# Performance work log

Hardware: AMD Instinct MI355X
Metric: run time of the kernel (lower is better)

Reference implementation:

```python
import jax, jax.numpy as jnp
import numpy as np

EPS = 1e-6
INV_T = 100.0
STEPS = 7  # eval_steps


def setup_inputs() -> dict:
    key = jax.random.key(0)
    k1, k2 = jax.random.split(key)
    B, C, H, W, R = 8, 512, 128, 128, 64
    x = jax.random.uniform(k1, (B, C, H, W), dtype=jnp.float32)
    bases = jax.random.uniform(k2, (B, C, R), dtype=jnp.float32)
    # _build_bases: F.normalize(bases, dim=1) -> L2 normalize over D
    bases = bases / jnp.maximum(jnp.linalg.norm(bases, axis=1, keepdims=True), 1e-12)
    return {"x": x, "bases": bases}


def _nmf(xf, bases):
    # xf: [B, D, N], bases: [B, D, R]
    # coef init: softmax(inv_t * x^T @ bases) over R
    coef = jax.nn.softmax(INV_T * jnp.einsum('bdn,bdr->bnr', xf, bases), axis=-1)

    def step(carry, _):
        bases, coef = carry
        # multiplicative update for coef: coef * (x^T B) / (coef (B^T B))
        num = jnp.einsum('bdn,bdr->bnr', xf, bases)          # [B,N,R]
        den = coef @ (jnp.swapaxes(bases, 1, 2) @ bases)      # [B,N,R]
        coef = coef * num / (den + EPS)
        # multiplicative update for bases: B * (x coef) / (B (coef^T coef))
        num = jnp.einsum('bdn,bnr->bdr', xf, coef)            # [B,D,R]
        den = bases @ (jnp.swapaxes(coef, 1, 2) @ coef)       # [B,D,R]
        bases = bases * num / (den + EPS)
        return (bases, coef), None

    (bases, coef), _ = jax.lax.scan(step, (bases, coef), None, length=STEPS)
    # compute_coef: one final coef update
    num = jnp.einsum('bdn,bdr->bnr', xf, bases)
    den = coef @ (jnp.swapaxes(bases, 1, 2) @ bases)
    coef = coef * num / (den + EPS)
    return bases, coef


def reference(x, bases):
    B, C, H, W = x.shape
    N = H * W
    xf = x.reshape(B, C, N)  # S=1, D=C
    bases, coef = _nmf(xf, bases)
    out = jnp.einsum('bdr,bnr->bdn', bases, coef)  # bases @ coef^T
    return out.reshape(B, C, H, W)
```

## Files before the change

kernel.cpp:

```cpp
#include <hip/hip_runtime.h>
#include <cstdint>
#include <cstddef>

namespace {

constexpr int B_ = 8;
constexpr int D_ = 512;
constexpr int N_ = 16384;
constexpr int R_ = 64;
constexpr float EPS_ = 1e-6f;
constexpr float INVT_ = 100.0f;

typedef __attribute__((ext_vector_type(4))) float f32x4;
typedef __attribute__((ext_vector_type(8))) short s16x8;
typedef __attribute__((ext_vector_type(4))) short s16x4;

#define MFMA16(A, Bv, C) __builtin_amdgcn_mfma_f32_16x16x32_bf16(A, Bv, C, 0, 0, 0)

#define VMW(n) asm volatile("s_waitcnt vmcnt(" #n ")" ::: "memory")
#define LGKM0 asm volatile("s_waitcnt lgkmcnt(0)" ::: "memory")
#define SCHEDB __builtin_amdgcn_sched_barrier(0)
#define BARRIER do { SCHEDB; __builtin_amdgcn_s_barrier(); SCHEDB; } while (0)

typedef __attribute__((address_space(3))) unsigned int lds_u32_t;
typedef const __attribute__((address_space(1))) unsigned int glb_u32_t;

__device__ __forceinline__ void gl2lds16(const void* g, void* l) {
    __builtin_amdgcn_global_load_lds((glb_u32_t*)g, (lds_u32_t*)l, 16, 0, 0);
}

__device__ __forceinline__ unsigned short f2bf(float x) {
    unsigned int u = __float_as_uint(x);
    return (unsigned short)((u + 0x7fffu + ((u >> 16) & 1u)) >> 16);
}
__device__ __forceinline__ float bf2f(unsigned short u) {
    return __uint_as_float(((unsigned int)u) << 16);
}
__device__ __forceinline__ s16x8 ld8(const unsigned short* p) {
    return *reinterpret_cast<const s16x8*>(p);
}

__device__ __forceinline__ void stage16(const unsigned short* __restrict__ rowbase,
        size_t rstride_elems, unsigned short* __restrict__ buf, int w, int lane) {
#pragma unroll
    for (int i = 0; i < 4; ++i) {
        int r = w * 4 + i;
        const char* src = reinterpret_cast<const char*>(rowbase + (size_t)r * rstride_elems)
                        + ((lane << 4) ^ ((r & 7) << 4));
        gl2lds16(src, reinterpret_cast<char*>(buf) + r * 1024);
    }
}
__device__ __forceinline__ s16x8 read_t16(const unsigned short* buf, int row, int ks, int h4) {
    return *reinterpret_cast<const s16x8*>(reinterpret_cast<const char*>(buf)
        + row * 1024 + ((ks * 64 + h4 * 16) ^ ((row & 7) << 4)));
}
__device__ __forceinline__ void stage_c16(const unsigned short* __restrict__ cnr_n0,
        unsigned short* __restrict__ buf, int w, int lane) {
    int h = w & 1;
    int row = h * 8 + (lane >> 3);
    const char* src = reinterpret_cast<const char*>(cnr_n0 + (size_t)row * R_)
                    + ((((lane & 7) ^ (row & 7))) << 4);
    gl2lds16(src, reinterpret_cast<char*>(buf) + h * 1024);
}
__device__ __forceinline__ s16x8 read_c16(const unsigned short* buf, int row, int ks, int h4) {
    return *reinterpret_cast<const s16x8*>(reinterpret_cast<const char*>(buf)
        + row * 128 + ((ks * 64 + h4 * 16) ^ ((row & 7) << 4)));
}
__device__ __forceinline__ float read_c_scalar(const unsigned short* buf, int row, int r) {
    return bf2f(*reinterpret_cast<const unsigned short*>(
        reinterpret_cast<const char*>(buf) + row * 128 + ((r * 2) ^ ((row & 7) << 4))));
}

__global__ __launch_bounds__(256) void k_convert(const float* __restrict__ X,
        unsigned short* __restrict__ Xhi, unsigned short* __restrict__ XThi,
        unsigned short* __restrict__ XTlo, int have_lo) {
    __shared__ float lds[64][65];
    int id = blockIdx.x;
    int nblk = id & 255, dblk = (id >> 8) & 7, b = id >> 11;
    int t = threadIdx.x;
    const float* Xb = X + ((size_t)b * D_ + dblk * 64) * N_ + (size_t)nblk * 64;
    {
        int d = t >> 2;
#pragma unroll
        for (int i = 0; i < 4; ++i) {
            int c = (t & 3) * 4 + i * 16;
            f32x4 v = *reinterpret_cast<const f32x4*>(Xb + (size_t)d * N_ + c);
#pragma unroll
            for (int k = 0; k < 4; ++k) lds[d][c + k] = v[k];
        }
    }
    __syncthreads();
    {
        int d = t >> 2, c0 = (t & 3) * 16;
        unsigned short* dst = Xhi + ((size_t)b * D_ + dblk * 64 + d) * N_ + (size_t)nblk * 64 + c0;
        s16x8 v0, v1;
#pragma unroll
        for (int k = 0; k < 8; ++k) {
            v0[k] = (short)f2bf(lds[d][c0 + k]);
            v1[k] = (short)f2bf(lds[d][c0 + 8 + k]);
        }
        *reinterpret_cast<s16x8*>(dst) = v0;
        *reinterpret_cast<s16x8*>(dst + 8) = v1;
    }
    {
        int n = t >> 2, c0 = (t & 3) * 16;
        size_t off = ((size_t)b * N_ + nblk * 64 + n) * D_ + dblk * 64 + c0;
        s16x8 h0, h1, l0, l1;
#pragma unroll
        for (int k = 0; k < 8; ++k) {
            float a = lds[c0 + k][n], c = lds[c0 + 8 + k][n];
            unsigned short ha = f2bf(a), hc = f2bf(c);
            h0[k] = (short)ha; h1[k] = (short)hc;
            l0[k] = (short)f2bf(a - bf2f(ha));
            l1[k] = (short)f2bf(c - bf2f(hc));
        }
        *reinterpret_cast<s16x8*>(XThi + off) = h0;
        *reinterpret_cast<s16x8*>(XThi + off + 8) = h1;
        if (have_lo) {
            *reinterpret_cast<s16x8*>(XTlo + off) = l0;
            *reinterpret_cast<s16x8*>(XTlo + off + 8) = l1;
        }
    }
}

__global__ __launch_bounds__(256) void k_ginit(const float* __restrict__ Bin,
        float* __restrict__ bases, unsigned short* __restrict__ BThi,
        unsigned short* __restrict__ BTlo) {
    __shared__ float lds[64][65];
    int id = blockIdx.x, dblk = id & 7, b = id >> 3;
    int t = threadIdx.x, tn = t & 63, tq = t >> 6;
    const float* Bb = Bin + ((size_t)b * D_ + dblk * 64) * R_;
    float* bb = bases + ((size_t)b * D_ + dblk * 64) * R_;
#pragma unroll
    for (int i = 0; i < 16; ++i) {
        int d = i * 4 + tq;
        float v = Bb[d * R_ + tn];
        lds[d][tn] = v;
        bb[d * R_ + tn] = v;
    }
    __syncthreads();
#pragma unroll
    for (int i = 0; i < 16; ++i) {
        int r = i * 4 + tq;
        float v = lds[tn][r];
        unsigned short hi = f2bf(v);
        size_t off = ((size_t)b * R_ + r) * D_ + dblk * 64 + tn;
        BThi[off] = hi;
        BTlo[off] = f2bf(v - bf2f(hi));
    }
}

__global__ __launch_bounds__(256) void k_gram(const unsigned short* __restrict__ BT,
        unsigned short* __restrict__ G) {
    int b = blockIdx.x;
    int t = threadIdx.x, lane = t & 63, w = t >> 6;
    int m16 = lane & 15, h4 = lane >> 4;
    const unsigned short* BTb = BT + (size_t)b * R_ * D_;
    f32x4 acc[4];
#pragma unroll
    for (int j = 0; j < 4; ++j) acc[j] = (f32x4){0.f, 0.f, 0.f, 0.f};
#pragma unroll
    for (int k0 = 0; k0 < D_; k0 += 32) {
        int kg = k0 + (h4 << 3);
        s16x8 frag[4];
#pragma unroll
        for (int j = 0; j < 4; ++j)
            frag[j] = ld8(BTb + (size_t)(j * 16 + m16) * D_ + kg);
        s16x8 fw = ld8(BTb + (size_t)(w * 16 + m16) * D_ + kg);
#pragma unroll
        for (int j = 0; j < 4; ++j) acc[j] = MFMA16(fw, frag[j], acc[j]);
    }
    unsigned short* Gb = G + (size_t)b * R_ * R_;
#pragma unroll
    for (int j = 0; j < 4; ++j)
#pragma unroll
        for (int q = 0; q < 4; ++q) {
            int r1 = 16 * w + (h4 << 2) + q;
            Gb[r1 * R_ + 16 * j + m16] = f2bf(acc[j][q]);
        }
}

template <int LO>
__global__ __launch_bounds__(256, 2) void k_init(const unsigned short* __restrict__ XThi,
        const unsigned short* __restrict__ XTlo, const unsigned short* __restrict__ BThi,
        const unsigned short* __restrict__ BTlo, const unsigned short* __restrict__ G,
        unsigned short* __restrict__ CTb, unsigned short* __restrict__ Cnr) {
    __shared__ __align__(16) unsigned short xhbuf[2][16 * 512];
    __shared__ __align__(16) unsigned short xlbuf[LO ? 2 : 1][16 * 512];
    __shared__ __align__(16) unsigned short ldsc[16 * 64];
    __shared__ float red[2][4][16];
    int id = blockIdx.x, blk = id & 63, b = id >> 6;
    int t = threadIdx.x, lane = t & 63, w = t >> 6;
    int m16 = lane & 15, h4 = lane >> 4;
    const unsigned short* XTb = XThi + (size_t)b * N_ * D_;
    const unsigned short* XLb = XTlo + (size_t)b * N_ * D_;
    const unsigned short* BThb = BThi + (size_t)b * R_ * D_;
    const unsigned short* BTlb = BTlo + (size_t)b * R_ * D_;
    const unsigned short* Gb = G + (size_t)b * R_ * R_;
    unsigned short* CTbb = CTb + (size_t)b * R_ * N_;
    unsigned short* Cnrb = Cnr + (size_t)b * N_ * R_;
    s16x8 abh[16], abl[16], g[2];
#pragma unroll
    for (int ks = 0; ks < 16; ++ks) {
        size_t off = (size_t)(w * 16 + m16) * D_ + ks * 32 + h4 * 8;
        abh[ks] = ld8(BThb + off);
        abl[ks] = ld8(BTlb + off);
    }
#pragma unroll
    for (int ks = 0; ks < 2; ++ks)
        g[ks] = ld8(Gb + (size_t)(w * 16 + m16) * R_ + ks * 32 + h4 * 8);
    SCHEDB;
    stage16(XTb + (size_t)(blk * 16 + 0) * 16 * D_, D_, xhbuf[0], w, lane);
    if (LO) stage16(XLb + (size_t)(blk * 16 + 0) * 16 * D_, D_, xlbuf[0], w, lane);
    stage16(XTb + (size_t)(blk * 16 + 1) * 16 * D_, D_, xhbuf[1], w, lane);
    if (LO) stage16(XLb + (size_t)(blk * 16 + 1) * 16 * D_, D_, xlbuf[1], w, lane);
    SCHEDB;

    int swz = (m16 & 7) << 4;
    char* crow = reinterpret_cast<char*>(ldsc) + m16 * 128;

    for (int tt = 0; tt < 16; ++tt) {
        int cur = tt & 1;
        int n0 = (blk * 16 + tt) * 16;
        if (LO) {
            if (tt == 0) VMW(8);
            else if (tt == 15) VMW(5);
            else VMW(13);
        } else {
            if (tt == 0) VMW(4);
            else if (tt == 15) VMW(5);
            else VMW(9);
        }
        BARRIER;
        const unsigned short* xh = xhbuf[cur];
        const unsigned short* xl = xlbuf[LO ? cur : 0];
        f32x4 acc = (f32x4){0.f, 0.f, 0.f, 0.f};
#pragma unroll
        for (int ks = 0; ks < 16; ++ks) {
            s16x8 bh = read_t16(xh, m16, ks, h4);
            acc = MFMA16(abh[ks], bh, acc);
            acc = MFMA16(abl[ks], bh, acc);
            if (LO) {
                s16x8 bl = read_t16(xl, m16, ks, h4);
                acc = MFMA16(abh[ks], bl, acc);
            }
        }
        float mx = fmaxf(fmaxf(acc[0], acc[1]), fmaxf(acc[2], acc[3]));
        mx = fmaxf(mx, __shfl_xor(mx, 16));
        mx = fmaxf(mx, __shfl_xor(mx, 32));
        if (lane < 16) red[0][w][m16] = mx;
        LGKM0; BARRIER;
        mx = fmaxf(fmaxf(red[0][0][m16], red[0][1][m16]),
                   fmaxf(red[0][2][m16], red[0][3][m16]));
        float p[4], ss = 0.f;
#pragma unroll
        for (int q = 0; q < 4; ++q) {
            p[q] = __expf(INVT_ * (acc[q] - mx));
            ss += p[q];
        }
        ss += __shfl_xor(ss, 16);
        ss += __shfl_xor(ss, 32);
        if (lane < 16) red[1][w][m16] = ss;
        LGKM0; BARRIER;
        ss = red[1][0][m16] + red[1][1][m16] + red[1][2][m16] + red[1][3][m16];
        float inv = 1.f / ss;
#pragma unroll
        for (int q = 0; q < 4; ++q) {
            int r = w * 16 + h4 * 4 + q;
            *reinterpret_cast<unsigned short*>(crow + ((r * 2) ^ swz)) = f2bf(p[q] * inv);
        }
        LGKM0; BARRIER;
        f32x4 dacc = (f32x4){0.f, 0.f, 0.f, 0.f};
#pragma unroll
        for (int ks = 0; ks < 2; ++ks) {
            s16x8 bf = *reinterpret_cast<const s16x8*>(crow + ((ks * 64 + h4 * 16) ^ swz));
            dacc = MFMA16(g[ks], bf, dacc);
        }
        s16x4 cn;
        float c1v[4];
#pragma unroll
        for (int q = 0; q < 4; ++q) {
            c1v[q] = p[q] * inv * acc[q] / (dacc[q] + EPS_);
            cn[q] = (short)f2bf(c1v[q]);
        }
        LGKM0; BARRIER;
        SCHEDB;
#pragma unroll
        for (int q = 0; q < 4; ++q)
            CTbb[(size_t)(w * 16 + h4 * 4 + q) * N_ + n0 + m16] = f2bf(c1v[q]);
        *reinterpret_cast<s16x4*>(Cnrb + (size_t)(n0 + m16) * R_ + w * 16 + h4 * 4) = cn;
        SCHEDB;
        if (tt + 2 < 16) {
            stage16(XTb + (size_t)(blk * 16 + tt + 2) * 16 * D_, D_, xhbuf[cur], w, lane);
            if (LO) stage16(XLb + (size_t)(blk * 16 + tt + 2) * 16 * D_, D_, xlbuf[cur], w, lane);
        }
        SCHEDB;
    }
}

__global__ __launch_bounds__(256, 4) void k_cu(const unsigned short* __restrict__ XThi,
        const unsigned short* __restrict__ BThi, const unsigned short* __restrict__ G,
        unsigned short* __restrict__ CTb, unsigned short* __restrict__ Cnr) {
    __shared__ __align__(16) unsigned short xbuf[2][16 * 512];
    __shared__ __align__(16) unsigned short cbuf[2][16 * 64];
    int id = blockIdx.x, blk = id & 127, b = id >> 7;
    int t = threadIdx.x, lane = t & 63, w = t >> 6;
    int m16 = lane & 15, h4 = lane >> 4;
    const unsigned short* XTb = XThi + (size_t)b * N_ * D_;
    const unsigned short* BTb = BThi + (size_t)b * R_ * D_;
    const unsigned short* Gb = G + (size_t)b * R_ * R_;
    unsigned short* CTbb = CTb + (size_t)b * R_ * N_;
    unsigned short* Cnrb = Cnr + (size_t)b * N_ * R_;
    s16x8 abt[16], g[2];
#pragma unroll
    for (int ks = 0; ks < 16; ++ks)
        abt[ks] = ld8(BTb + (size_t)(w * 16 + m16) * D_ + ks * 32 + h4 * 8);
#pragma unroll
    for (int ks = 0; ks < 2; ++ks)
        g[ks] = ld8(Gb + (size_t)(w * 16 + m16) * R_ + ks * 32 + h4 * 8);
    SCHEDB;
    stage16(XTb + (size_t)(blk * 8 + 0) * 16 * D_, D_, xbuf[0], w, lane);
    stage_c16(Cnrb + (size_t)(blk * 8 + 0) * 16 * R_, cbuf[0], w, lane);
    stage16(XTb + (size_t)(blk * 8 + 1) * 16 * D_, D_, xbuf[1], w, lane);
    stage_c16(Cnrb + (size_t)(blk * 8 + 1) * 16 * R_, cbuf[1], w, lane);
    SCHEDB;

    for (int tt = 0; tt < 8; ++tt) {
        int cur = tt & 1;
        int n0 = (blk * 8 + tt) * 16;
        if (tt == 0) VMW(5);
        else if (tt == 7) VMW(5);
        else VMW(10);
        BARRIER;
        const unsigned short* xb = xbuf[cur];
        const unsigned short* cb = cbuf[cur];
        f32x4 acc = (f32x4){0.f, 0.f, 0.f, 0.f};
#pragma unroll
        for (int ks = 0; ks < 16; ++ks)
            acc = MFMA16(abt[ks], read_t16(xb, m16, ks, h4), acc);
        f32x4 dacc = (f32x4){0.f, 0.f, 0.f, 0.f};
#pragma unroll
        for (int ks = 0; ks < 2; ++ks)
            dacc = MFMA16(g[ks], read_c16(cb, m16, ks, h4), dacc);
        s16x4 cn;
        float c1v[4];
#pragma unroll
        for (int q = 0; q < 4; ++q) {
            int r = w * 16 + h4 * 4 + q;
            float cold = read_c_scalar(cb, m16, r);
            c1v[q] = cold * acc[q] / (dacc[q] + EPS_);
            cn[q] = (short)f2bf(c1v[q]);
        }
        LGKM0; BARRIER;
        SCHEDB;
#pragma unroll
        for (int q = 0; q < 4; ++q)
            CTbb[(size_t)(w * 16 + h4 * 4 + q) * N_ + n0 + m16] = f2bf(c1v[q]);
        *reinterpret_cast<s16x4*>(Cnrb + (size_t)(n0 + m16) * R_ + w * 16 + h4 * 4) = cn;
        SCHEDB;
        if (tt + 2 < 8) {
            stage16(XTb + (size_t)(blk * 8 + tt + 2) * 16 * D_, D_, xbuf[cur], w, lane);
            stage_c16(Cnrb + (size_t)(blk * 8 + tt + 2) * 16 * R_, cbuf[cur], w, lane);
        }
        SCHEDB;
    }
}

__global__ __launch_bounds__(256, 4) void k_bu1t(const unsigned short* __restrict__ Xhi,
        const unsigned short* __restrict__ CTb, unsigned short* __restrict__ wsN2) {
    __shared__ __align__(16) unsigned short xbuf[2][16 * 512];
    int id = blockIdx.x;
    int b = id >> 7, c = (id >> 2) & 31, dg = id & 3;
    int t = threadIdx.x, lane = t & 63, w = t >> 6;
    int m16 = lane & 15, h4 = lane >> 4;
    const unsigned short* Xb = Xhi + (size_t)b * D_ * N_ + c * 512;
    const unsigned short* Cbc = CTb + (size_t)b * R_ * N_ + c * 512;
    s16x8 act[16];
#pragma unroll
    for (int ks = 0; ks < 16; ++ks)
        act[ks] = ld8(Cbc + (size_t)(w * 16 + m16) * N_ + ks * 32 + h4 * 8);
    SCHEDB;
    stage16(Xb + (size_t)(dg * 128 + 0) * N_, N_, xbuf[0], w, lane);
    stage16(Xb + (size_t)(dg * 128 + 16) * N_, N_, xbuf[1], w, lane);
    SCHEDB;
    unsigned short* n2 = wsN2 + (size_t)(b * 32 + c) * R_ * D_;
    for (int tt = 0; tt < 8; ++tt) {
        int cur = tt & 1;
        int d0 = dg * 128 + tt * 16;
        if (tt == 0) VMW(4);
        else if (tt == 7) VMW(4);
        else VMW(8);
        BARRIER;
        const unsigned short* xb = xbuf[cur];
        f32x4 acc = (f32x4){0.f, 0.f, 0.f, 0.f};
#pragma unroll
        for (int ks = 0; ks < 16; ++ks)
            acc = MFMA16(act[ks], read_t16(xb, m16, ks, h4), acc);
        LGKM0; BARRIER;
        SCHEDB;
        if (tt + 2 < 8)
            stage16(Xb + (size_t)(dg * 128 + (tt + 2) * 16) * N_, N_, xbuf[cur], w, lane);
        SCHEDB;
#pragma unroll
        for (int q = 0; q < 4; ++q)
            n2[(size_t)(w * 16 + h4 * 4 + q) * D_ + d0 + m16] = f2bf(acc[q]);
        SCHEDB;
    }
}

__global__ __launch_bounds__(256) void k_hg(const unsigned short* __restrict__ CTb,
        float* __restrict__ wsH) {
    int id = blockIdx.x, c = id & 31, b = id >> 5;
    int t = threadIdx.x, lane = t & 63, w = t >> 6;
    int m16 = lane & 15, h4 = lane >> 4;
    const unsigned short* Cb = CTb + (size_t)b * R_ * N_ + c * 512;
    f32x4 hacc[4];
#pragma unroll
    for (int j = 0; j < 4; ++j) hacc[j] = (f32x4){0.f, 0.f, 0.f, 0.f};
#pragma unroll
    for (int ks = 0; ks < 16; ++ks) {
        int kg = ks * 32 + h4 * 8;
        s16x8 bj[4];
#pragma unroll
        for (int j = 0; j < 4; ++j) bj[j] = ld8(Cb + (size_t)(j * 16 + m16) * N_ + kg);
        s16x8 aw = ld8(Cb + (size_t)(w * 16 + m16) * N_ + kg);
#pragma unroll
        for (int j = 0; j < 4; ++j) hacc[j] = MFMA16(aw, bj[j], hacc[j]);
    }
    float* Hp = wsH + (size_t)(b * 32 + c) * R_ * R_;
#pragma unroll
    for (int j = 0; j < 4; ++j)
#pragma unroll
        for (int q = 0; q < 4; ++q)
            Hp[(w * 16 + (h4 << 2) + q) * R_ + j * 16 + m16] = hacc[j][q];
}

__global__ __launch_bounds__(256) void k_hred(const float* __restrict__ wsH,
        float* __restrict__ Hf) {
    int id = blockIdx.x, q = id & 3, b = id >> 2;
    int t = threadIdx.x;
    int i = q * 1024 + t * 4;
    f32x4 s = (f32x4){0.f, 0.f, 0.f, 0.f};
    for (int c = 0; c < 32; ++c)
        s += *reinterpret_cast<const f32x4*>(wsH + ((size_t)b * 32 + c) * 4096 + i);
    *reinterpret_cast<f32x4*>(Hf + (size_t)b * 4096 + i) = s;
}

__global__ __launch_bounds__(256) void k_bu2(const unsigned short* __restrict__ wsN2,
        const float* __restrict__ Hf, float* __restrict__ bases,
        unsigned short* __restrict__ BThi, unsigned short* __restrict__ Bdr) {
    __shared__ float ldsH[64][64];
    __shared__ float ldsb[16][65];
    __shared__ float ldsn[16][65];
    int id = blockIdx.x, dblk = id & 31, b = id >> 5;
    int t = threadIdx.x;
    int d0 = dblk * 16;
    const float* Hb = Hf + (size_t)b * 4096;
#pragma unroll
    for (int i = 0; i < 4; ++i) {
        f32x4 v = *reinterpret_cast<const f32x4*>(Hb + i * 1024 + t * 4);
        *reinterpret_cast<f32x4*>(&ldsH[0][0] + i * 1024 + t * 4) = v;
    }
    {
        int d = t >> 4, p0 = (t & 15) * 4;
        f32x4 v = *reinterpret_cast<const f32x4*>(bases + ((size_t)b * D_ + d0 + d) * R_ + p0);
#pragma unroll
        for (int k = 0; k < 4; ++k) ldsb[d][p0 + k] = v[k];
    }
    __syncthreads();
#pragma unroll
    for (int j = 0; j < 4; ++j) {
        int i = t + 256 * j;
        int r = i >> 4, d = i & 15;
        float n2 = 0.f;
        for (int c = 0; c < 32; ++c)
            n2 += bf2f(wsN2[(((size_t)b * 32 + c) * R_ + r) * D_ + d0 + d]);
        float den = 0.f;
#pragma unroll 8
        for (int p = 0; p < 64; ++p) den += ldsb[d][p] * ldsH[p][r];
        ldsn[d][r] = ldsb[d][r] * n2 / (den + EPS_);
    }
    __syncthreads();
    {
        int d = t >> 4, r0 = (t & 15) * 4;
        f32x4 v;
        s16x4 hv;
#pragma unroll
        for (int k = 0; k < 4; ++k) {
            v[k] = ldsn[d][r0 + k];
            hv[k] = (short)f2bf(v[k]);
        }
        *reinterpret_cast<f32x4*>(bases + ((size_t)b * D_ + d0 + d) * R_ + r0) = v;
        *reinterpret_cast<s16x4*>((unsigned short*)Bdr + ((size_t)b * D_ + d0 + d) * R_ + r0) = hv;
    }
    {
        int r = t >> 2, dd = (t & 3) * 4;
        s16x4 hv;
#pragma unroll
        for (int k = 0; k < 4; ++k) hv[k] = (short)f2bf(ldsn[dd + k][r]);
        *reinterpret_cast<s16x4*>(BThi + ((size_t)b * R_ + r) * D_ + d0 + dd) = hv;
    }
}

__global__ __launch_bounds__(256, 2) void k_out(const unsigned short* __restrict__ Bdr,
        const unsigned short* __restrict__ Cnr, float* __restrict__ Out) {
    __shared__ float ldso[4][64 * 68 + 8];
    int id = blockIdx.x, nblk = id & 63, dblk = (id >> 6) & 7, b = id >> 9;
    int t = threadIdx.x, lane = t & 63, w = t >> 6;
    int m16 = lane & 15, h4 = lane >> 4;
    const unsigned short* Bb = Bdr + (size_t)b * D_ * R_;
    const unsigned short* Cb = Cnr + (size_t)b * N_ * R_;
    int d0 = dblk * 64, n0 = nblk * 256 + w * 64;
    f32x4 acc[4][4];
#pragma unroll
    for (int i = 0; i < 4; ++i)
#pragma unroll
        for (int j = 0; j < 4; ++j) acc[i][j] = (f32x4){0.f, 0.f, 0.f, 0.f};
#pragma unroll
    for (int k0 = 0; k0 < 64; k0 += 32) {
        int kg = k0 + (h4 << 3);
        s16x8 afrag[4], bfrag[4];
#pragma unroll
        for (int i = 0; i < 4; ++i)
            afrag[i] = ld8(Bb + (size_t)(d0 + i * 16 + m16) * R_ + kg);
#pragma unroll
        for (int j = 0; j < 4; ++j)
            bfrag[j] = ld8(Cb + (size_t)(n0 + j * 16 + m16) * R_ + kg);
#pragma unroll
        for (int i = 0; i < 4; ++i)
#pragma unroll
            for (int j = 0; j < 4; ++j)
                acc[i][j] = MFMA16(afrag[i], bfrag[j], acc[i][j]);
    }
#pragma unroll
    for (int i = 0; i < 4; ++i)
#pragma unroll
        for (int j = 0; j < 4; ++j)
#pragma unroll
            for (int q = 0; q < 4; ++q)
                ldso[w][(i * 16 + h4 * 4 + q) * 68 + j * 16 + m16] = acc[i][j][q];
    __syncthreads();
    float* Ob = Out + (size_t)b * D_ * N_ + (size_t)d0 * N_ + nblk * 256;
    int quad = lane >> 4, cc = (lane & 15) * 4;
#pragma unroll
    for (int i = 0; i < 16; ++i) {
        int d = w * 16 + i;
        f32x4 v = *reinterpret_cast<const f32x4*>(&ldso[quad][d * 68 + cc]);
        *reinterpret_cast<f32x4*>(Ob + (size_t)d * N_ + quad * 64 + cc) = v;
    }
}

}

extern "C" void kernel_launch(void* const* d_in, const int* in_sizes, int n_in,
                              void* d_out, int out_size, void* d_ws, size_t ws_size,
                              hipStream_t stream) {
    const float* X = (const float*)d_in[0];
    const float* Bin = (const float*)d_in[1];
    float* Out = (float*)d_out;
    char* ws = (char*)d_ws;

    const size_t o_Xhi  = 0;
    const size_t o_XThi = o_Xhi  + (size_t)B_ * D_ * N_ * 2;
    const size_t o_CTb  = o_XThi + (size_t)B_ * N_ * D_ * 2;
    const size_t o_Cnr  = o_CTb  + (size_t)B_ * R_ * N_ * 2;
    const size_t o_bas  = o_Cnr  + (size_t)B_ * N_ * R_ * 2;
    const size_t o_BThi = o_bas  + (size_t)B_ * D_ * R_ * 4;
    const size_t o_BTlo = o_BThi + (size_t)B_ * R_ * D_ * 2;
    const size_t o_Bdr  = o_BTlo + (size_t)B_ * R_ * D_ * 2;
    const size_t o_G    = o_Bdr  + (size_t)B_ * D_ * R_ * 2;
    const size_t o_H    = o_G    + (size_t)B_ * R_ * R_ * 2;
    const size_t o_Hf   = o_H    + (size_t)B_ * 32 * R_ * R_ * 4;
    const size_t o_N2   = o_Hf   + (size_t)B_ * R_ * R_ * 4;
    const size_t BASE   = o_N2   + (size_t)B_ * 32 * R_ * D_ * 2;
    const size_t o_XTlo = BASE;
    const size_t FULL   = o_XTlo + (size_t)B_ * N_ * D_ * 2;

    if (ws_size < BASE) return;
    int have_lo = ws_size >= FULL ? 1 : 0;

    unsigned short* Xhi  = (unsigned short*)(ws + o_Xhi);
    unsigned short* XThi = (unsigned short*)(ws + o_XThi);
    unsigned short* XTlo = (unsigned short*)(ws + (have_lo ? o_XTlo : o_XThi));
    unsigned short* CTb  = (unsigned short*)(ws + o_CTb);
    unsigned short* Cnr  = (unsigned short*)(ws + o_Cnr);
    float*          bas  = (float*)(ws + o_bas);
    unsigned short* BThi = (unsigned short*)(ws + o_BThi);
    unsigned short* BTlo = (unsigned short*)(ws + o_BTlo);
    unsigned short* Bdr  = (unsigned short*)(ws + o_Bdr);
    unsigned short* G    = (unsigned short*)(ws + o_G);
    float*          H    = (float*)(ws + o_H);
    float*          Hf   = (float*)(ws + o_Hf);
    unsigned short* N2   = (unsigned short*)(ws + o_N2);

    k_convert<<<dim3(16384), dim3(256), 0, stream>>>(X, Xhi, XThi, XTlo, have_lo);
    k_ginit<<<dim3(64), dim3(256), 0, stream>>>(Bin, bas, BThi, BTlo);
    k_gram<<<dim3(8), dim3(256), 0, stream>>>(BThi, G);
    if (have_lo)
        k_init<1><<<dim3(512), dim3(256), 0, stream>>>(XThi, XTlo, BThi, BTlo, G, CTb, Cnr);
    else
        k_init<0><<<dim3(512), dim3(256), 0, stream>>>(XThi, XTlo, BThi, BTlo, G, CTb, Cnr);
    for (int s = 0; s < 7; ++s) {
        k_bu1t<<<dim3(1024), dim3(256), 0, stream>>>(Xhi, CTb, N2);
        k_hg<<<dim3(256), dim3(256), 0, stream>>>(CTb, H);
        k_hred<<<dim3(32), dim3(256), 0, stream>>>(H, Hf);
        k_bu2<<<dim3(256), dim3(256), 0, stream>>>(N2, Hf, bas, BThi, Bdr);
        k_gram<<<dim3(8), dim3(256), 0, stream>>>(BThi, G);
        k_cu<<<dim3(1024), dim3(256), 0, stream>>>(XThi, BThi, G, CTb, Cnr);
    }
    k_out<<<dim3(4096), dim3(256), 0, stream>>>(Bdr, Cnr, Out);
}
```

Measured before the change: 1.238 ms.

## Fuse coef Gram into bases-numerator kernel and rework convert LDS swizzle

```diff
diff --git a/kernel.cpp b/kernel.cpp
--- a/kernel.cpp
+++ b/kernel.cpp
@@ -74,46 +74,50 @@
 __global__ __launch_bounds__(256) void k_convert(const float* __restrict__ X,
         unsigned short* __restrict__ Xhi, unsigned short* __restrict__ XThi,
         unsigned short* __restrict__ XTlo, int have_lo) {
-    __shared__ float lds[64][65];
+    __shared__ f32x4 lds4[64 * 16];
     int id = blockIdx.x;
     int nblk = id & 255, dblk = (id >> 8) & 7, b = id >> 11;
     int t = threadIdx.x;
+    int d = t >> 2, c0 = (t & 3) * 16;
     const float* Xb = X + ((size_t)b * D_ + dblk * 64) * N_ + (size_t)nblk * 64;
+    f32x4 v[4];
+#pragma unroll
+    for (int i = 0; i < 4; ++i)
+        v[i] = *reinterpret_cast<const f32x4*>(Xb + (size_t)d * N_ + c0 + 4 * i);
     {
-        int d = t >> 2;
-#pragma unroll
-        for (int i = 0; i < 4; ++i) {
-            int c = (t & 3) * 4 + i * 16;
-            f32x4 v = *reinterpret_cast<const f32x4*>(Xb + (size_t)d * N_ + c);
-#pragma unroll
-            for (int k = 0; k < 4; ++k) lds[d][c + k] = v[k];
-        }
+        int swz = (d ^ (d >> 3)) & 7;
+#pragma unroll
+        for (int i = 0; i < 4; ++i)
+            lds4[d * 16 + ((((t & 3) << 2) + i) ^ swz)] = v[i];
+    }
+    {
+        unsigned short* dst = Xhi + ((size_t)b * D_ + dblk * 64 + d) * N_
+                            + (size_t)nblk * 64 + c0;
+        s16x8 h0, h1;
+#pragma unroll
+        for (int k = 0; k < 8; ++k) {
+            h0[k] = (short)f2bf(v[k >> 2][k & 3]);
+            h1[k] = (short)f2bf(v[2 + (k >> 2)][k & 3]);
+        }
+        *reinterpret_cast<s16x8*>(dst) = h0;
+        *reinterpret_cast<s16x8*>(dst + 8) = h1;
     }
     __syncthreads();
     {
-        int d = t >> 2, c0 = (t & 3) * 16;
-        unsigned short* dst = Xhi + ((size_t)b * D_ + dblk * 64 + d) * N_ + (size_t)nblk * 64 + c0;
-        s16x8 v0, v1;
-#pragma unroll
-        for (int k = 0; k < 8; ++k) {
-            v0[k] = (short)f2bf(lds[d][c0 + k]);
-            v1[k] = (short)f2bf(lds[d][c0 + 8 + k]);
-        }
-        *reinterpret_cast<s16x8*>(dst) = v0;
-        *reinterpret_cast<s16x8*>(dst + 8) = v1;
-    }
-    {
-        int n = t >> 2, c0 = (t & 3) * 16;
+        int n = t >> 2;
+        const float* L = reinterpret_cast<const float*>(lds4);
+        s16x8 h0, h1, l0, l1;
+#pragma unroll
+        for (int k = 0; k < 16; ++k) {
+            int r = c0 + k;
+            int sz = (r ^ (r >> 3)) & 7;
+            float a = L[r * 64 + ((((n >> 2) ^ sz) << 2) | (n & 3))];
+            unsigned short ha = f2bf(a);
+            unsigned short la = f2bf(a - bf2f(ha));
+            if (k < 8) { h0[k] = (short)ha; l0[k] = (short)la; }
+            else       { h1[k - 8] = (short)ha; l1[k - 8] = (short)la; }
+        }
         size_t off = ((size_t)b * N_ + nblk * 64 + n) * D_ + dblk * 64 + c0;
-        s16x8 h0, h1, l0, l1;
-#pragma unroll
-        for (int k = 0; k < 8; ++k) {
-            float a = lds[c0 + k][n], c = lds[c0 + 8 + k][n];
-            unsigned short ha = f2bf(a), hc = f2bf(c);
-            h0[k] = (short)ha; h1[k] = (short)hc;
-            l0[k] = (short)f2bf(a - bf2f(ha));
-            l1[k] = (short)f2bf(c - bf2f(hc));
-        }
         *reinterpret_cast<s16x8*>(XThi + off) = h0;
         *reinterpret_cast<s16x8*>(XThi + off + 8) = h1;
         if (have_lo) {
@@ -367,7 +371,8 @@
 }
 
 __global__ __launch_bounds__(256, 4) void k_bu1t(const unsigned short* __restrict__ Xhi,
-        const unsigned short* __restrict__ CTb, unsigned short* __restrict__ wsN2) {
+        const unsigned short* __restrict__ CTb, unsigned short* __restrict__ wsN2,
+        float* __restrict__ wsH) {
     __shared__ __align__(16) unsigned short xbuf[2][16 * 512];
     int id = blockIdx.x;
     int b = id >> 7, c = (id >> 2) & 31, dg = id & 3;
@@ -379,6 +384,21 @@
 #pragma unroll
     for (int ks = 0; ks < 16; ++ks)
         act[ks] = ld8(Cbc + (size_t)(w * 16 + m16) * N_ + ks * 32 + h4 * 8);
+    f32x4 hacc = (f32x4){0.f, 0.f, 0.f, 0.f};
+    {
+        const unsigned short* Hrow = Cbc + (size_t)(dg * 16 + m16) * N_;
+#pragma unroll
+        for (int gg = 0; gg < 4; ++gg) {
+            SCHEDB;
+            s16x8 hb[4];
+#pragma unroll
+            for (int j = 0; j < 4; ++j)
+                hb[j] = ld8(Hrow + (gg * 4 + j) * 32 + h4 * 8);
+#pragma unroll
+            for (int j = 0; j < 4; ++j)
+                hacc = MFMA16(act[gg * 4 + j], hb[j], hacc);
+        }
+    }
     SCHEDB;
     stage16(Xb + (size_t)(dg * 128 + 0) * N_, N_, xbuf[0], w, lane);
     stage16(Xb + (size_t)(dg * 128 + 16) * N_, N_, xbuf[1], w, lane);
@@ -406,33 +426,10 @@
             n2[(size_t)(w * 16 + h4 * 4 + q) * D_ + d0 + m16] = f2bf(acc[q]);
         SCHEDB;
     }
-}
-
-__global__ __launch_bounds__(256) void k_hg(const unsigned short* __restrict__ CTb,
-        float* __restrict__ wsH) {
-    int id = blockIdx.x, c = id & 31, b = id >> 5;
-    int t = threadIdx.x, lane = t & 63, w = t >> 6;
-    int m16 = lane & 15, h4 = lane >> 4;
-    const unsigned short* Cb = CTb + (size_t)b * R_ * N_ + c * 512;
-    f32x4 hacc[4];
-#pragma unroll
-    for (int j = 0; j < 4; ++j) hacc[j] = (f32x4){0.f, 0.f, 0.f, 0.f};
-#pragma unroll
-    for (int ks = 0; ks < 16; ++ks) {
-        int kg = ks * 32 + h4 * 8;
-        s16x8 bj[4];
-#pragma unroll
-        for (int j = 0; j < 4; ++j) bj[j] = ld8(Cb + (size_t)(j * 16 + m16) * N_ + kg);
-        s16x8 aw = ld8(Cb + (size_t)(w * 16 + m16) * N_ + kg);
-#pragma unroll
-        for (int j = 0; j < 4; ++j) hacc[j] = MFMA16(aw, bj[j], hacc[j]);
-    }
-    float* Hp = wsH + (size_t)(b * 32 + c) * R_ * R_;
-#pragma unroll
-    for (int j = 0; j < 4; ++j)
-#pragma unroll
-        for (int q = 0; q < 4; ++q)
-            Hp[(w * 16 + (h4 << 2) + q) * R_ + j * 16 + m16] = hacc[j][q];
+    float* Hp = wsH + (size_t)(b * 32 + c) * 4096;
+#pragma unroll
+    for (int q = 0; q < 4; ++q)
+        Hp[(w * 16 + h4 * 4 + q) * R_ + dg * 16 + m16] = hacc[q];
 }
 
 __global__ __launch_bounds__(256) void k_hred(const float* __restrict__ wsH,
@@ -601,8 +598,7 @@
     else
         k_init<0><<<dim3(512), dim3(256), 0, stream>>>(XThi, XTlo, BThi, BTlo, G, CTb, Cnr);
     for (int s = 0; s < 7; ++s) {
-        k_bu1t<<<dim3(1024), dim3(256), 0, stream>>>(Xhi, CTb, N2);
-        k_hg<<<dim3(256), dim3(256), 0, stream>>>(CTb, H);
+        k_bu1t<<<dim3(1024), dim3(256), 0, stream>>>(Xhi, CTb, N2, H);
         k_hred<<<dim3(32), dim3(256), 0, stream>>>(H, Hf);
         k_bu2<<<dim3(256), dim3(256), 0, stream>>>(N2, Hf, bas, BThi, Bdr);
         k_gram<<<dim3(8), dim3(256), 0, stream>>>(BThi, G);
```

New measurement: 1.222 ms. Within noise of the previous version (-1.2%).
